# Kernel tuning notes

Measured on AMD Instinct MI355X. Metric: run time of the kernel, lower is better.

## Reference

```python
import jax, jax.numpy as jnp
import numpy as np

EPS = 1e-7  # K.epsilon()

def squash(s, axis=-1):
    # v = (||s||^2 / (1 + ||s||^2)) * s / ||s||
    sq = jnp.sum(jnp.square(s), axis=axis, keepdims=True)
    scale = sq / (1.0 + sq) / jnp.sqrt(sq + EPS)
    return scale * s

def setup_inputs() -> dict:
    key = jax.random.key(0)
    k1, k2, k3 = jax.random.split(key, 3)
    B, J, P = 128, 2048, 8      # batch, input_num_capsule, input_dim_capsule
    N, D = 32, 16               # num_capsule, dim_capsule
    x = jax.random.normal(k1, (B, J, P), dtype=jnp.float32)
    W = jax.random.normal(k2, (N, J, D, P), dtype=jnp.float32) * 0.1
    bias = jax.random.normal(k3, (N, D), dtype=jnp.float32) * 0.1
    return {"x": x, "W": W, "bias": bias}

def reference(x, W, bias):
    # x: [B, J, P], W: [N, J, D, P], bias: [N, D]
    routings = 3
    # inputs_hat[b,n,j,d] = sum_p W[n,j,d,p] * x[b,j,p]   -> [B, N, J, D]
    u_hat = jnp.einsum('njdp,bjp->bnjd', W, x)
    B_, N, J, _ = u_hat.shape
    b = jnp.zeros((B_, N, J), dtype=u_hat.dtype)
    outputs = None
    for i in range(routings):
        c = jax.nn.softmax(b, axis=1)                      # coupling over output caps
        s = jnp.einsum('bnj,bnjd->bnd', c, u_hat) + bias   # weighted sum + bias
        outputs = squash(s)                                # [B, N, D]
        if i < routings - 1:
            b = b + jnp.einsum('bnd,bnjd->bnj', outputs, u_hat)  # agreement
    return outputs
```

## Files before the change

kernel.cpp:

```cpp
#include <hip/hip_runtime.h>
#include <hip/hip_bf16.h>

#define B_   128
#define J_   2048
#define N_   32
#define D_   16
#define NJC  32

typedef __attribute__((ext_vector_type(8))) short short8b;
typedef __attribute__((ext_vector_type(4))) float f32x4;
typedef __attribute__((ext_vector_type(16))) float f32x16;

__device__ inline short bf16s(float f) {
    union { __hip_bfloat16 h; short s; } u;
    u.h = __float2bfloat16(f);
    return u.s;
}


__global__ __launch_bounds__(256) void capsW(const float* __restrict__ W,
                                             __hip_bfloat16* __restrict__ Wbf,
                                             __hip_bfloat16* __restrict__ Wt) {
    __shared__ float lds[16 * 132];
    const int t = threadIdx.x;
    const size_t base = (size_t)blockIdx.x * 2048;
    const int r  = t >> 4;
    const int e0 = (t & 15) * 8;

    float4 a = *(const float4*)(W + base + t * 8);
    float4 b = *(const float4*)(W + base + t * 8 + 4);
    short8b w8;
    w8[0]=bf16s(a.x); w8[1]=bf16s(a.y); w8[2]=bf16s(a.z); w8[3]=bf16s(a.w);
    w8[4]=bf16s(b.x); w8[5]=bf16s(b.y); w8[6]=bf16s(b.z); w8[7]=bf16s(b.w);
    *(short8b*)((short*)Wbf + base + t * 8) = w8;
    *(float4*)&lds[r * 132 + e0]     = a;
    *(float4*)&lds[r * 132 + e0 + 4] = b;
    __syncthreads();

    short8b o8;
    #pragma unroll
    for (int k = 0; k < 8; ++k) {
        int q = e0 + k;
        int p = q >> 4, d = q & 15;
        o8[k] = bf16s(lds[r * 132 + d * 8 + p]);
    }
    *(short8b*)((short*)Wt + base + t * 8) = o8;
}

__global__ __launch_bounds__(256) void capsT(const float* __restrict__ x,
                                             float* __restrict__ xT) {
    __shared__ float tile[32 * 260 + 4];
    const int t  = threadIdx.x;
    const int jt = blockIdx.x & 63;
    const int bt = blockIdx.x >> 6;
    const int j0 = jt * 32, b0 = bt * 32;

    for (int idx = t; idx < 2048; idx += 256) {
        int bl = idx >> 6, f4 = idx & 63;
        float4 v = *(const float4*)(x + (size_t)(b0 + bl) * 16384 + j0 * 8 + f4 * 4);
        *(float4*)&tile[bl * 260 + f4 * 4] = v;
    }
    __syncthreads();
    for (int idx = t; idx < 2048; idx += 256) {
        int jj = idx >> 6, f4o = idx & 63;
        int bl = f4o >> 1, po = (f4o & 1) * 4;
        float4 v = *(const float4*)&tile[bl * 260 + jj * 8 + po];
        *(float4*)(xT + ((size_t)(j0 + jj) * 128 + b0 + bl) * 8 + po) = v;
    }
}

__global__ __launch_bounds__(256) void capsA(const __hip_bfloat16* __restrict__ Wbf,
                                             const float* __restrict__ xT,
                                             const __hip_bfloat16* __restrict__ cT,
                                             float* __restrict__ s_part,
                                             int mode) {
    const int t     = threadIdx.x;
    const int lane  = t & 63;
    const int i     = blockIdx.x;
    const int jc    = (i & 7) + 8 * (i >> 8);
    const int n     = (i >> 3) & 31;
    const int wv    = t >> 6;
    const int colid = lane & 15;
    const int kgrp  = lane >> 4;

    const int b0 = wv * 32 + colid;
    const int b1 = b0 + 16;

    f32x4 acc0 = {0.f, 0.f, 0.f, 0.f};
    f32x4 acc1 = {0.f, 0.f, 0.f, 0.f};

    for (int ks = 0; ks < 16; ++ks) {
        const int j = jc * 64 + ks * 4 + kgrp;

        short8b bfrag = *(const short8b*)((const short*)Wbf
                          + (((size_t)n * J_ + j) * 16 + colid) * 8);

        float c0 = 1.0f / 32.0f, c1 = 1.0f / 32.0f;
        if (mode) {
            c0 = __bfloat162float(cT[((size_t)n * J_ + j) * B_ + b0]);
            c1 = __bfloat162float(cT[((size_t)n * J_ + j) * B_ + b1]);
        }

        const float4* xp0 = (const float4*)(xT + ((size_t)j * 128 + b0) * 8);
        float4 xa = xp0[0], xb = xp0[1];
        short8b afrag0;
        afrag0[0] = bf16s(xa.x * c0); afrag0[1] = bf16s(xa.y * c0);
        afrag0[2] = bf16s(xa.z * c0); afrag0[3] = bf16s(xa.w * c0);
        afrag0[4] = bf16s(xb.x * c0); afrag0[5] = bf16s(xb.y * c0);
        afrag0[6] = bf16s(xb.z * c0); afrag0[7] = bf16s(xb.w * c0);

        const float4* xp1 = (const float4*)(xT + ((size_t)j * 128 + b1) * 8);
        float4 xe = xp1[0], xf = xp1[1];
        short8b afrag1;
        afrag1[0] = bf16s(xe.x * c1); afrag1[1] = bf16s(xe.y * c1);
        afrag1[2] = bf16s(xe.z * c1); afrag1[3] = bf16s(xe.w * c1);
        afrag1[4] = bf16s(xf.x * c1); afrag1[5] = bf16s(xf.y * c1);
        afrag1[6] = bf16s(xf.z * c1); afrag1[7] = bf16s(xf.w * c1);

        acc0 = __builtin_amdgcn_mfma_f32_16x16x32_bf16(afrag0, bfrag, acc0, 0, 0, 0);
        acc1 = __builtin_amdgcn_mfma_f32_16x16x32_bf16(afrag1, bfrag, acc1, 0, 0, 0);
    }

    float* sdst = s_part + (size_t)jc * (B_ * N_ * D_);
    #pragma unroll
    for (int r = 0; r < 4; ++r) {
        int brow = wv * 32 + kgrp * 4 + r;
        sdst[(size_t)brow * 512 + n * 16 + colid]        = acc0[r];
        sdst[(size_t)(brow + 16) * 512 + n * 16 + colid] = acc1[r];
    }
}

__global__ __launch_bounds__(256) void capsR(const float* __restrict__ s_part,
                                             const float* __restrict__ bias,
                                             float* __restrict__ out,
                                             __hip_bfloat16* __restrict__ oT) {
    int gid = blockIdx.x * 256 + threadIdx.x;
    float sv = bias[gid & 511];
    #pragma unroll
    for (int jc = 0; jc < NJC; ++jc)
        sv += s_part[(size_t)jc * 65536 + gid];
    float sq = sv * sv;
    sq += __shfl_xor(sq, 1);
    sq += __shfl_xor(sq, 2);
    sq += __shfl_xor(sq, 4);
    sq += __shfl_xor(sq, 8);
    float scale = sq / (1.0f + sq) / sqrtf(sq + 1e-7f);
    float ov = scale * sv;
    out[gid] = ov;
    int b = gid >> 9, nd = gid & 511;
    int n = nd >> 4, d = nd & 15;
    oT[((size_t)n * B_ + b) * D_ + d] = __float2bfloat16(ov);
}

__global__ __launch_bounds__(256) void capsB(const __hip_bfloat16* __restrict__ Wt,
                                             const float* __restrict__ xT,
                                             const __hip_bfloat16* __restrict__ oT,
                                             __hip_bfloat16* __restrict__ blogT,
                                             int accumulate) {
    const int t    = threadIdx.x;
    const int lane = t & 63;
    const int i    = blockIdx.x;
    const int xcd  = i & 7;
    const int r    = i >> 3;
    const int jq   = xcd * 64 + (r & 63);
    const int nh   = r >> 6;
    const int j0   = jq * 4;
    const int wv   = t >> 6;
    const int g    = lane >> 5;
    const int col  = lane & 31;
    const int jl   = col >> 3;
    const int p    = col & 7;
    const int bt   = wv;

    float4 xv[4];
    #pragma unroll
    for (int jl2 = 0; jl2 < 4; ++jl2)
        xv[jl2] = *(const float4*)(xT + ((size_t)(j0 + jl2) * 128 + bt * 32 + col) * 8 + g * 4);

    f32x16 zz;
    #pragma unroll
    for (int q = 0; q < 16; ++q) zz[q] = 0.0f;

    #pragma unroll 2
    for (int nn = 0; nn < 16; ++nn) {
        const int n = nh * 16 + nn;

        short8b bfrag = *(const short8b*)(oT + ((size_t)n * B_ + bt * 32 + col) * D_ + g * 8);

        short8b afrag = *(const short8b*)((const short*)Wt
                          + (((size_t)n * J_ + j0 + jl) * 8 + p) * 16 + g * 8);

        f32x16 acc =
            __builtin_amdgcn_mfma_f32_32x32x16_bf16(afrag, bfrag, zz, 0, 0, 0);

        const int b = bt * 32 + col;
        #pragma unroll
        for (int jl2 = 0; jl2 < 4; ++jl2) {
            const int j = j0 + jl2;
            float4 v = xv[jl2];
            float tt = acc[jl2 * 4 + 0] * v.x
                     + acc[jl2 * 4 + 1] * v.y
                     + acc[jl2 * 4 + 2] * v.z
                     + acc[jl2 * 4 + 3] * v.w;
            tt += __shfl_xor(tt, 32);
            if (g == (jl2 >> 1)) {
                size_t a0 = ((size_t)n * J_ + j) * B_ + b;
                if (accumulate) tt += __bfloat162float(blogT[a0]);
                blogT[a0] = __float2bfloat16(tt);
            }
        }
    }
}

__global__ __launch_bounds__(256) void capsD(const __hip_bfloat16* __restrict__ blogT,
                                             __hip_bfloat16* __restrict__ cT) {
    int gid = blockIdx.x * 256 + threadIdx.x;
    float v[32];
    float m = -1e30f;
    #pragma unroll
    for (int nn = 0; nn < 32; ++nn) {
        v[nn] = __bfloat162float(blogT[(size_t)nn * (J_ * B_) + gid]);
        m = fmaxf(m, v[nn]);
    }
    float sum = 0.0f;
    #pragma unroll
    for (int nn = 0; nn < 32; ++nn) sum += __expf(v[nn] - m);
    float inv = 1.0f / sum;
    #pragma unroll
    for (int nn = 0; nn < 32; ++nn)
        cT[(size_t)nn * (J_ * B_) + gid] = __float2bfloat16(__expf(v[nn] - m) * inv);
}

extern "C" void kernel_launch(void* const* d_in, const int* in_sizes, int n_in,
                              void* d_out, int out_size, void* d_ws, size_t ws_size,
                              hipStream_t stream) {
    const float* x    = (const float*)d_in[0];
    const float* W    = (const float*)d_in[1];
    const float* bias = (const float*)d_in[2];
    float* out = (float*)d_out;

    float* ws = (float*)d_ws;
    float*           xT     = ws;
    __hip_bfloat16*  blogT  = (__hip_bfloat16*)(ws + 2097152);
    __hip_bfloat16*  cT     = (__hip_bfloat16*)(ws + 6291456);
    float*           s_part = ws + 10485760;
    __hip_bfloat16*  oT     = (__hip_bfloat16*)(ws + 12582912);
    __hip_bfloat16*  Wbf    = (__hip_bfloat16*)(ws + 12615680);
    __hip_bfloat16*  Wt     = (__hip_bfloat16*)(ws + 16809984);

    dim3 b256(256);

    capsW<<<dim3(4096), b256, 0, stream>>>(W, Wbf, Wt);
    capsT<<<dim3(256),  b256, 0, stream>>>(x, xT);

    capsA<<<dim3(1024), b256, 0, stream>>>(Wbf, xT, cT, s_part, 0);
    capsR<<<dim3(256),  b256, 0, stream>>>(s_part, bias, out, oT);
    capsB<<<dim3(1024), b256, 0, stream>>>(Wt, xT, oT, blogT, 0);

    capsD<<<dim3(1024), b256, 0, stream>>>(blogT, cT);
    capsA<<<dim3(1024), b256, 0, stream>>>(Wbf, xT, cT, s_part, 1);
    capsR<<<dim3(256),  b256, 0, stream>>>(s_part, bias, out, oT);
    capsB<<<dim3(1024), b256, 0, stream>>>(Wt, xT, oT, blogT, 1);

    capsD<<<dim3(1024), b256, 0, stream>>>(blogT, cT);
    capsA<<<dim3(1024), b256, 0, stream>>>(Wbf, xT, cT, s_part, 1);
    capsR<<<dim3(256),  b256, 0, stream>>>(s_part, bias, out, oT);
}
```

Measured before the change: 141.2 us.

## Fuse softmax into agreement kernel by covering all capsules per block

The agreement kernel now loops over all 32 output capsules per block instead of splitting them across two blocks. Each thread keeps the logits in registers and computes the softmax over capsules directly, writing the coupling coefficients. This removes the separate softmax kernel and its read of the logits. The final iteration also skips writing logits that are never used again. In exchange the grid is halved, the serial loop per block is twice as long, and register pressure rises from the 64-entry keep array.

```diff
diff --git a/kernel.cpp b/kernel.cpp
--- a/kernel.cpp
+++ b/kernel.cpp
@@ -156,47 +156,43 @@
                                              const float* __restrict__ xT,
                                              const __hip_bfloat16* __restrict__ oT,
                                              __hip_bfloat16* __restrict__ blogT,
-                                             int accumulate) {
+                                             __hip_bfloat16* __restrict__ cT,
+                                             int accumulate, int writeBlog) {
     const int t    = threadIdx.x;
     const int lane = t & 63;
     const int i    = blockIdx.x;
     const int xcd  = i & 7;
-    const int r    = i >> 3;
-    const int jq   = xcd * 64 + (r & 63);
-    const int nh   = r >> 6;
+    const int jq   = xcd * 64 + (i >> 3);
     const int j0   = jq * 4;
     const int wv   = t >> 6;
     const int g    = lane >> 5;
     const int col  = lane & 31;
     const int jl   = col >> 3;
     const int p    = col & 7;
-    const int bt   = wv;
+    const int b    = wv * 32 + col;
 
     float4 xv[4];
     #pragma unroll
     for (int jl2 = 0; jl2 < 4; ++jl2)
-        xv[jl2] = *(const float4*)(xT + ((size_t)(j0 + jl2) * 128 + bt * 32 + col) * 8 + g * 4);
+        xv[jl2] = *(const float4*)(xT + ((size_t)(j0 + jl2) * 128 + b) * 8 + g * 4);
 
     f32x16 zz;
     #pragma unroll
     for (int q = 0; q < 16; ++q) zz[q] = 0.0f;
 
-    #pragma unroll 2
-    for (int nn = 0; nn < 16; ++nn) {
-        const int n = nh * 16 + nn;
-
-        short8b bfrag = *(const short8b*)(oT + ((size_t)n * B_ + bt * 32 + col) * D_ + g * 8);
-
+    float keep[2][32];
+
+    #pragma unroll
+    for (int nn = 0; nn < 32; ++nn) {
+        short8b bfrag = *(const short8b*)(oT + ((size_t)nn * B_ + b) * D_ + g * 8);
         short8b afrag = *(const short8b*)((const short*)Wt
-                          + (((size_t)n * J_ + j0 + jl) * 8 + p) * 16 + g * 8);
+                          + (((size_t)nn * J_ + j0 + jl) * 8 + p) * 16 + g * 8);
 
         f32x16 acc =
             __builtin_amdgcn_mfma_f32_32x32x16_bf16(afrag, bfrag, zz, 0, 0, 0);
 
-        const int b = bt * 32 + col;
         #pragma unroll
         for (int jl2 = 0; jl2 < 4; ++jl2) {
-            const int j = j0 + jl2;
             float4 v = xv[jl2];
             float tt = acc[jl2 * 4 + 0] * v.x
                      + acc[jl2 * 4 + 1] * v.y
@@ -204,31 +200,32 @@
                      + acc[jl2 * 4 + 3] * v.w;
             tt += __shfl_xor(tt, 32);
             if (g == (jl2 >> 1)) {
-                size_t a0 = ((size_t)n * J_ + j) * B_ + b;
+                size_t a0 = ((size_t)nn * J_ + j0 + jl2) * B_ + b;
                 if (accumulate) tt += __bfloat162float(blogT[a0]);
-                blogT[a0] = __float2bfloat16(tt);
+                if (writeBlog)  blogT[a0] = __float2bfloat16(tt);
+                keep[jl2 & 1][nn] = tt;
             }
         }
     }
-}
-
-__global__ __launch_bounds__(256) void capsD(const __hip_bfloat16* __restrict__ blogT,
-                                             __hip_bfloat16* __restrict__ cT) {
-    int gid = blockIdx.x * 256 + threadIdx.x;
-    float v[32];
-    float m = -1e30f;
-    #pragma unroll
-    for (int nn = 0; nn < 32; ++nn) {
-        v[nn] = __bfloat162float(blogT[(size_t)nn * (J_ * B_) + gid]);
-        m = fmaxf(m, v[nn]);
-    }
-    float sum = 0.0f;
-    #pragma unroll
-    for (int nn = 0; nn < 32; ++nn) sum += __expf(v[nn] - m);
-    float inv = 1.0f / sum;
-    #pragma unroll
-    for (int nn = 0; nn < 32; ++nn)
-        cT[(size_t)nn * (J_ * B_) + gid] = __float2bfloat16(__expf(v[nn] - m) * inv);
+
+    #pragma unroll
+    for (int k2 = 0; k2 < 2; ++k2) {
+        const int j = j0 + 2 * g + k2;
+        float m = keep[k2][0];
+        #pragma unroll
+        for (int nn = 1; nn < 32; ++nn) m = fmaxf(m, keep[k2][nn]);
+        float sum = 0.0f;
+        #pragma unroll
+        for (int nn = 0; nn < 32; ++nn) {
+            float e = __expf(keep[k2][nn] - m);
+            keep[k2][nn] = e;
+            sum += e;
+        }
+        float inv = 1.0f / sum;
+        #pragma unroll
+        for (int nn = 0; nn < 32; ++nn)
+            cT[((size_t)nn * J_ + j) * B_ + b] = __float2bfloat16(keep[k2][nn] * inv);
+    }
 }
 
 extern "C" void kernel_launch(void* const* d_in, const int* in_sizes, int n_in,
@@ -255,14 +252,12 @@
 
     capsA<<<dim3(1024), b256, 0, stream>>>(Wbf, xT, cT, s_part, 0);
     capsR<<<dim3(256),  b256, 0, stream>>>(s_part, bias, out, oT);
-    capsB<<<dim3(1024), b256, 0, stream>>>(Wt, xT, oT, blogT, 0);
-
-    capsD<<<dim3(1024), b256, 0, stream>>>(blogT, cT);
+    capsB<<<dim3(512),  b256, 0, stream>>>(Wt, xT, oT, blogT, cT, 0, 1);
+
     capsA<<<dim3(1024), b256, 0, stream>>>(Wbf, xT, cT, s_part, 1);
     capsR<<<dim3(256),  b256, 0, stream>>>(s_part, bias, out, oT);
-    capsB<<<dim3(1024), b256, 0, stream>>>(Wt, xT, oT, blogT, 1);
-
-    capsD<<<dim3(1024), b256, 0, stream>>>(blogT, cT);
+    capsB<<<dim3(512),  b256, 0, stream>>>(Wt, xT, oT, blogT, cT, 1, 0);
+
     capsA<<<dim3(1024), b256, 0, stream>>>(Wbf, xT, cT, s_part, 1);
     capsR<<<dim3(256),  b256, 0, stream>>>(s_part, bias, out, oT);
 }
```

After: 160.8 us. 1.14x slower.
